# Optimization experiments

Measured on AMD Instinct MI355X. Metric: run time of the kernel, lower is better.

Reference implementation:

```python
import math
import jax, jax.numpy as jnp
import numpy as np

GROUPS = 8
EPS = 1e-5


def setup_inputs() -> dict:
    key = jax.random.key(0)
    ks = jax.random.split(key, 4)
    B, C, H, W = 4, 128, 64, 64
    x = jax.random.normal(ks[0], (B, C, H, W), dtype=jnp.float32)
    norm_w = jnp.ones((C,), dtype=jnp.float32)
    norm_b = jnp.zeros((C,), dtype=jnp.float32)
    qkv_w = jax.random.normal(ks[1], (3 * C, C), dtype=jnp.float32) * 0.02
    qkv_b = jnp.zeros((3 * C,), dtype=jnp.float32)
    proj_w = jax.random.normal(ks[2], (C, C), dtype=jnp.float32) * 0.02
    proj_b = jnp.zeros((C,), dtype=jnp.float32)
    return {"x": x, "norm_w": norm_w, "norm_b": norm_b,
            "qkv_w": qkv_w, "qkv_b": qkv_b,
            "proj_w": proj_w, "proj_b": proj_b}


def reference(x, norm_w, norm_b, qkv_w, qkv_b, proj_w, proj_b):
    B, C, H, W = x.shape
    N = H * W
    # GroupNorm over (C/G, H, W) per group
    xr = x.reshape(B, GROUPS, C // GROUPS, N)
    mean = xr.mean(axis=(2, 3), keepdims=True)
    var = xr.var(axis=(2, 3), keepdims=True)
    h = ((xr - mean) * jax.lax.rsqrt(var + EPS)).reshape(B, C, N)
    h = h * norm_w[None, :, None] + norm_b[None, :, None]
    # 1x1 conv QKV == per-pixel linear: [B, 3C, N]
    qkv = jnp.einsum('oc,bcn->bon', qkv_w, h) + qkv_b[None, :, None]
    q, k, v = jnp.split(qkv, 3, axis=1)  # each [B, C, N]
    scale = 1.0 / math.sqrt(C)
    attn = jax.nn.softmax(jnp.einsum('bci,bcj->bij', q, k) * scale, axis=-1)  # [B,N,N]
    out = jnp.einsum('bij,bcj->bci', attn, v)  # [B, C, N]
    proj = jnp.einsum('oc,bcn->bon', proj_w, out) + proj_b[None, :, None]
    return x + proj.reshape(B, C, H, W)
```

## Files before the change

kernel.cpp:

```cpp
#include <hip/hip_runtime.h>

typedef float  f32x4   __attribute__((ext_vector_type(4)));
typedef float  f32x16  __attribute__((ext_vector_type(16)));
typedef short  bf16x8  __attribute__((ext_vector_type(8)));
typedef unsigned short u16;

constexpr int B_ = 4;
constexpr int C_ = 128;
constexpr int N_ = 4096;
constexpr int G_ = 8;
constexpr int CperG = 16;
constexpr float EPS_ = 1e-5f;
constexpr float SCALE_ = 0.08838834764831845f;

__device__ inline u16 f2bf(float f) {
    union { float f; unsigned u; } v; v.f = f;
    unsigned r = v.u + 0x7fffu + ((v.u >> 16) & 1u);
    return (u16)(r >> 16);
}
__device__ inline unsigned pk2(float a, float b) {
    return (unsigned)f2bf(a) | ((unsigned)f2bf(b) << 16);
}

__global__ __launch_bounds__(256) void prep_kernel(const float* __restrict__ x,
                                                   const float* __restrict__ qw,
                                                   const float* __restrict__ pw,
                                                   float* __restrict__ stats2,
                                                   u16* __restrict__ qwbf,
                                                   u16* __restrict__ pwbf) {
    int blk = blockIdx.x;
    if (blk < 256) {
        __shared__ float rs[4], rss[4];
        int bg = blk >> 3, chunk = blk & 7;
        const float4* xp = (const float4*)(x + (size_t)bg * (CperG * N_)) + chunk * 2048;
        float s = 0.f, ss = 0.f;
        for (int i = threadIdx.x; i < 2048; i += 256) {
            float4 v = xp[i];
            s  += v.x + v.y + v.z + v.w;
            ss += v.x*v.x + v.y*v.y + v.z*v.z + v.w*v.w;
        }
        #pragma unroll
        for (int off = 32; off > 0; off >>= 1) {
            s  += __shfl_down(s, off);
            ss += __shfl_down(ss, off);
        }
        int wv = threadIdx.x >> 6, ln = threadIdx.x & 63;
        if (ln == 0) { rs[wv] = s; rss[wv] = ss; }
        __syncthreads();
        if (threadIdx.x == 0) {
            stats2[blk*2]     = rs[0] + rs[1] + rs[2] + rs[3];
            stats2[blk*2 + 1] = rss[0] + rss[1] + rss[2] + rss[3];
        }
    } else {
        int fidx = ((blk - 256) * 256 + threadIdx.x) * 4;
        float4 v;
        u16* dst;
        if (fidx < 3*C_*C_) { v = *(const float4*)(qw + fidx); dst = qwbf + fidx; }
        else { int j = fidx - 3*C_*C_; v = *(const float4*)(pw + j); dst = pwbf + j; }
        ushort4 o;
        o.x = f2bf(v.x); o.y = f2bf(v.y); o.z = f2bf(v.z); o.w = f2bf(v.w);
        *(ushort4*)dst = o;
    }
}

constexpr int HS = 136;

__global__ __launch_bounds__(256, 2) void qkv_kernel(const float* __restrict__ x,
                                                     const float* __restrict__ stats2,
                                                     const float* __restrict__ nw,
                                                     const float* __restrict__ nb,
                                                     const u16* __restrict__ qwbf,
                                                     const float* __restrict__ qb,
                                                     u16* __restrict__ Qt,
                                                     u16* __restrict__ Ksw,
                                                     u16* __restrict__ Vsw,
                                                     float* __restrict__ qn2,
                                                     int* __restrict__ kmaxI) {
    int n0 = (blockIdx.x & 63) * 64;
    int b  = blockIdx.x >> 6;
    __shared__ u16 hs[64 * HS];
    __shared__ u16 Wl[64 * HS];
    __shared__ float gmean[8], grstd[8];
    int t = threadIdx.x;
    const float invM = 1.f / (float)(CperG * N_);
    if (t < 8) {
        const float* sp = stats2 + (size_t)(b*G_ + t)*16;
        float S = 0.f, SS = 0.f;
        #pragma unroll
        for (int k2 = 0; k2 < 8; ++k2) { S += sp[k2*2]; SS += sp[k2*2 + 1]; }
        float mean = S * invM;
        gmean[t] = mean;
        grstd[t] = rsqrtf(SS * invM - mean*mean + EPS_);
    }
    __syncthreads();
    #pragma unroll
    for (int r = 0; r < 8; ++r) {
        int idx = t + (r << 8);
        int c = idx >> 4, n4 = idx & 15;
        int g = c >> 4;
        float wgt = nw[c] * grstd[g];
        float bia = nb[c] - gmean[g] * wgt;
        float4 xv = *(const float4*)(x + ((size_t)(b*C_ + c))*N_ + n0 + n4*4);
        int base = (n4*4) * HS + c;
        hs[base         ] = f2bf(xv.x*wgt + bia);
        hs[base +     HS] = f2bf(xv.y*wgt + bia);
        hs[base + 2 * HS] = f2bf(xv.z*wgt + bia);
        hs[base + 3 * HS] = f2bf(xv.w*wgt + bia);
    }
    __syncthreads();
    int w = t >> 6, lane = t & 63, lo = lane & 15, hi = lane >> 4;
    bf16x8 hf[4];
    #pragma unroll
    for (int ch = 0; ch < 4; ++ch)
        hf[ch] = *(const bf16x8*)(hs + (16*w + lo)*HS + 32*ch + 8*hi);

    int Tb = (n0 >> 5) + (w >> 1);
    float nq = 0.f, nk = 0.f;
    for (int ck = 0; ck < 6; ++ck) {
        {
            int r = t >> 2, p = t & 3;
            const u16* src = qwbf + (size_t)(ck*64 + r)*C_ + p*32;
            u16* dst = Wl + r*HS + p*32;
            #pragma unroll
            for (int k2 = 0; k2 < 4; ++k2)
                *(uint4*)(dst + 8*k2) = *(const uint4*)(src + 8*k2);
        }
        __syncthreads();
        #pragma unroll
        for (int ot = 0; ot < 4; ++ot) {
            int o16 = ck*64 + ot*16;
            bf16x8 wf[4];
            #pragma unroll
            for (int ch = 0; ch < 4; ++ch)
                wf[ch] = *(const bf16x8*)(Wl + (ot*16 + lo)*HS + 32*ch + 8*hi);
            if (o16 < 2*C_) {
                f32x4 acc = (f32x4){0.f, 0.f, 0.f, 0.f};
                #pragma unroll
                for (int ch = 0; ch < 4; ++ch)
                    acc = __builtin_amdgcn_mfma_f32_16x16x32_bf16(wf[ch], hf[ch], acc, 0, 0, 0);
                float4 bv = *(const float4*)(qb + o16 + 4*hi);
                int n = n0 + 16*w + lo;
                ushort4 o4;
                if (o16 < C_) {
                    float q0 = (acc[0] + bv.x) * SCALE_;
                    float q1 = (acc[1] + bv.y) * SCALE_;
                    float q2 = (acc[2] + bv.z) * SCALE_;
                    float q3 = (acc[3] + bv.w) * SCALE_;
                    nq += (q0*q0 + q1*q1) + (q2*q2 + q3*q3);
                    o4.x = f2bf(q0); o4.y = f2bf(q1); o4.z = f2bf(q2); o4.w = f2bf(q3);
                    *(ushort4*)(Qt + ((size_t)b*N_ + n)*C_ + o16 + 4*hi) = o4;
                } else {
                    float k0 = acc[0] + bv.x, k1 = acc[1] + bv.y;
                    float k2 = acc[2] + bv.z, k3 = acc[3] + bv.w;
                    nk += (k0*k0 + k1*k1) + (k2*k2 + k3*k3);
                    o4.x = f2bf(k0); o4.y = f2bf(k1); o4.z = f2bf(k2); o4.w = f2bf(k3);
                    int cc = (o16 - C_) >> 4;
                    int lp = (16*(w & 1) + lo) + 32*(hi >> 1);
                    size_t fb = ((size_t)(b*128 + Tb)*8 + cc)*512;
                    *(ushort4*)(Ksw + fb + lp*8 + 4*(hi & 1)) = o4;
                }
            } else {
                f32x4 acc = (f32x4){0.f, 0.f, 0.f, 0.f};
                #pragma unroll
                for (int ch = 0; ch < 4; ++ch)
                    acc = __builtin_amdgcn_mfma_f32_16x16x32_bf16(hf[ch], wf[ch], acc, 0, 0, 0);
                float bia = qb[o16 + lo];
                ushort4 o4;
                o4.x = f2bf(acc[0] + bia);
                o4.y = f2bf(acc[1] + bia);
                o4.z = f2bf(acc[2] + bia);
                o4.w = f2bf(acc[3] + bia);
                int m  = (o16 - 2*C_) >> 4;
                int ct = m >> 1;
                int lp = (16*(m & 1) + lo) + 32*(hi & 1);
                size_t fb = (((size_t)(b*4 + ct)*128 + Tb)*2 + (w & 1))*512;
                *(ushort4*)(Vsw + fb + lp*8 + 4*(hi >> 1)) = o4;
            }
        }
        __syncthreads();
    }
    nq += __shfl_xor(nq, 16); nq += __shfl_xor(nq, 32);
    nk += __shfl_xor(nk, 16); nk += __shfl_xor(nk, 32);
    if (lane < 16) qn2[(size_t)b*N_ + n0 + 16*w + lo] = nq;
    #pragma unroll
    for (int off = 1; off < 16; off <<= 1)
        nk = fmaxf(nk, __shfl_xor(nk, off));
    if (lane == 0) atomicMax(&kmaxI[b], __float_as_int(nk));
}

__global__ __launch_bounds__(512, 2) void attn_kernel(const u16* __restrict__ Qt,
                                                      const u16* __restrict__ Ksw,
                                                      const u16* __restrict__ Vsw,
                                                      const float* __restrict__ qn2,
                                                      const int* __restrict__ kmaxI,
                                                      const u16* __restrict__ pwbf,
                                                      const float* __restrict__ pb,
                                                      const float* __restrict__ x,
                                                      float* __restrict__ out) {
    int lb = blockIdx.x;
    int b  = lb & 3;
    int i0 = 64 * (lb >> 2);
    int t = threadIdx.x;
    int w = t >> 6, lane = t & 63;
    int l31 = lane & 31, h = lane >> 5;
    int qt = w >> 2, ks = w & 3;

    __shared__ float Ob[64 * 132];
    __shared__ float lW[8][32];

    float kmax = sqrtf(__int_as_float(kmaxI[b]));
    float mq = sqrtf(qn2[(size_t)b*N_ + i0 + 32*qt + l31]) * kmax * 1.02f + 1e-6f;

    const u16* Qb = Qt + (size_t)b*N_*C_;
    bf16x8 qf[8];
    #pragma unroll
    for (int cc = 0; cc < 8; ++cc)
        qf[cc] = *(const bf16x8*)(Qb + (size_t)(i0 + 32*qt + l31)*C_ + 16*cc + 8*h);

    f32x16 acc[4];
    #pragma unroll
    for (int ct = 0; ct < 4; ++ct)
        #pragma unroll
        for (int r = 0; r < 16; ++r) acc[ct][r] = 0.f;
    float psum = 0.f;

    const u16* Kbase = Ksw + ((size_t)(b*128 + ks*32)*8)*512;
    bf16x8 kf[8], kn[8];
    #pragma unroll
    for (int cc = 0; cc < 8; ++cc)
        kf[cc] = *(const bf16x8*)(Kbase + cc*512 + lane*8);

    for (int it = 0; it < 32; ++it) {
        f32x16 s;
        #pragma unroll
        for (int r = 0; r < 16; ++r) s[r] = 0.f;
        #pragma unroll
        for (int cc = 0; cc < 8; ++cc)
            s = __builtin_amdgcn_mfma_f32_32x32x16_bf16(kf[cc], qf[cc], s, 0, 0, 0);
        {
            const u16* Kn = Kbase + ((size_t)(((it + 1) & 31))*8)*512;
            #pragma unroll
            for (int cc = 0; cc < 8; ++cc)
                kn[cc] = *(const bf16x8*)(Kn + cc*512 + lane*8);
        }
        int T = ks*32 + it;
        bf16x8 v1[4], v2[4];
        #pragma unroll
        for (int ct = 0; ct < 4; ++ct) {
            const u16* vb = Vsw + (((size_t)(b*4 + ct)*128 + T)*2)*512;
            v1[ct] = *(const bf16x8*)(vb + lane*8);
            v2[ct] = *(const bf16x8*)(vb + 512 + lane*8);
        }
        float p[16];
        #pragma unroll
        for (int r = 0; r < 16; ++r) {
            p[r] = __expf(s[r] - mq);
            psum += p[r];
        }
        union { bf16x8 v; unsigned u[4]; } pf1, pf2;
        pf1.u[0] = pk2(p[0],  p[1]);  pf1.u[1] = pk2(p[2],  p[3]);
        pf1.u[2] = pk2(p[4],  p[5]);  pf1.u[3] = pk2(p[6],  p[7]);
        pf2.u[0] = pk2(p[8],  p[9]);  pf2.u[1] = pk2(p[10], p[11]);
        pf2.u[2] = pk2(p[12], p[13]); pf2.u[3] = pk2(p[14], p[15]);
        #pragma unroll
        for (int ct = 0; ct < 4; ++ct) {
            acc[ct] = __builtin_amdgcn_mfma_f32_32x32x16_bf16(v1[ct], pf1.v, acc[ct], 0, 0, 0);
            acc[ct] = __builtin_amdgcn_mfma_f32_32x32x16_bf16(v2[ct], pf2.v, acc[ct], 0, 0, 0);
        }
        #pragma unroll
        for (int cc = 0; cc < 8; ++cc) kf[cc] = kn[cc];
    }

    psum += __shfl_xor(psum, 32);
    if (lane < 32) lW[w][l31] = psum;
    for (int i = 0; i < 4; ++i) {
        if (ks == i) {
            int q = 32*qt + l31;
            #pragma unroll
            for (int ct = 0; ct < 4; ++ct)
                #pragma unroll
                for (int qd = 0; qd < 4; ++qd) {
                    int c = 32*ct + 8*qd + 4*h;
                    float4 vv;
                    vv.x = acc[ct][4*qd + 0];
                    vv.y = acc[ct][4*qd + 1];
                    vv.z = acc[ct][4*qd + 2];
                    vv.w = acc[ct][4*qd + 3];
                    if (i == 0) {
                        *(float4*)(Ob + q*132 + c) = vv;
                    } else {
                        float4 o = *(const float4*)(Ob + q*132 + c);
                        o.x += vv.x; o.y += vv.y; o.z += vv.z; o.w += vv.w;
                        *(float4*)(Ob + q*132 + c) = o;
                    }
                }
        }
        __syncthreads();
    }
    int lo = lane & 15, hi = lane >> 4;
    int qtile = w >> 1, os = w & 1;
    int q = 16*qtile + lo;
    int qg = 4*(q >> 5), qc = q & 31;
    float linv = 1.f / (lW[qg][qc] + lW[qg+1][qc] + lW[qg+2][qc] + lW[qg+3][qc]);
    bf16x8 aa[4];
    #pragma unroll
    for (int ch = 0; ch < 4; ++ch) {
        float4 ua = *(const float4*)(Ob + q*132 + 32*ch + 8*hi);
        float4 ub = *(const float4*)(Ob + q*132 + 32*ch + 8*hi + 4);
        union { bf16x8 hh; unsigned u[4]; } pkd;
        pkd.u[0] = pk2(ua.x*linv, ua.y*linv);
        pkd.u[1] = pk2(ua.z*linv, ua.w*linv);
        pkd.u[2] = pk2(ub.x*linv, ub.y*linv);
        pkd.u[3] = pk2(ub.z*linv, ub.w*linv);
        aa[ch] = pkd.hh;
    }
    #pragma unroll
    for (int ot = 0; ot < 4; ++ot) {
        int ob = 64*os + 16*ot;
        f32x4 pr = (f32x4){0.f, 0.f, 0.f, 0.f};
        #pragma unroll
        for (int ch = 0; ch < 4; ++ch) {
            bf16x8 bw = *(const bf16x8*)(pwbf + (size_t)(ob + lo)*C_ + 32*ch + 8*hi);
            pr = __builtin_amdgcn_mfma_f32_16x16x32_bf16(aa[ch], bw, pr, 0, 0, 0);
        }
        int o = ob + lo;
        float pbv = pb[o];
        size_t base = ((size_t)(b*C_ + o))*N_ + i0 + 16*qtile + 4*hi;
        float4 xr = *(const float4*)(x + base);
        float4 res;
        res.x = xr.x + pr[0] + pbv;
        res.y = xr.y + pr[1] + pbv;
        res.z = xr.z + pr[2] + pbv;
        res.w = xr.w + pr[3] + pbv;
        *(float4*)(out + base) = res;
    }
}

extern "C" void kernel_launch(void* const* d_in, const int* in_sizes, int n_in,
                              void* d_out, int out_size, void* d_ws, size_t ws_size,
                              hipStream_t stream) {
    const float* x  = (const float*)d_in[0];
    const float* nw = (const float*)d_in[1];
    const float* nb = (const float*)d_in[2];
    const float* qw = (const float*)d_in[3];
    const float* qb = (const float*)d_in[4];
    const float* pw = (const float*)d_in[5];
    const float* pb = (const float*)d_in[6];
    float* out = (float*)d_out;

    char* p = (char*)d_ws;
    float* stats2 = (float*)p;                 p += 2048;
    float* qn2    = (float*)p;                 p += (size_t)B_*N_*4;
    int*   kmaxI  = (int*)p;                   p += 256;
    u16*   qwbf   = (u16*)p;                   p += (size_t)3*C_*C_*2;
    u16*   pwbf   = (u16*)p;                   p += (size_t)C_*C_*2;
    u16*   Qt     = (u16*)p;                   p += (size_t)B_*N_*C_*2;
    u16*   Ksw    = (u16*)p;                   p += (size_t)B_*N_*C_*2;
    u16*   Vsw    = (u16*)p;

    prep_kernel<<<dim3(320), 256, 0, stream>>>(x, qw, pw, stats2, qwbf, pwbf);
    qkv_kernel<<<dim3(256), 256, 0, stream>>>(x, stats2, nw, nb, qwbf, qb,
                                              Qt, Ksw, Vsw, qn2, kmaxI);
    attn_kernel<<<dim3(256), 512, 0, stream>>>(Qt, Ksw, Vsw, qn2, kmaxI,
                                               pwbf, pb, x, out);
}
```

Measured before the change: 153.9 us.

## Split QKV projection across sections, prefetch V, use hardware bf16 pack and exp2

```diff
diff --git a/kernel.cpp b/kernel.cpp
--- a/kernel.cpp
+++ b/kernel.cpp
@@ -11,15 +11,17 @@
 constexpr int G_ = 8;
 constexpr int CperG = 16;
 constexpr float EPS_ = 1e-5f;
-constexpr float SCALE_ = 0.08838834764831845f;
+constexpr float SCALE2_ = 0.08838834764831845f * 1.4426950408889634f;
 
 __device__ inline u16 f2bf(float f) {
     union { float f; unsigned u; } v; v.f = f;
     unsigned r = v.u + 0x7fffu + ((v.u >> 16) & 1u);
     return (u16)(r >> 16);
 }
-__device__ inline unsigned pk2(float a, float b) {
-    return (unsigned)f2bf(a) | ((unsigned)f2bf(b) << 16);
+__device__ inline unsigned cvtpk(float lo, float hi) {
+    unsigned r;
+    asm("v_cvt_pk_bf16_f32 %0, %1, %2" : "=v"(r) : "v"(lo), "v"(hi));
+    return r;
 }
 
 __global__ __launch_bounds__(256) void prep_kernel(const float* __restrict__ x,
@@ -65,7 +67,7 @@
 
 constexpr int HS = 136;
 
-__global__ __launch_bounds__(256, 2) void qkv_kernel(const float* __restrict__ x,
+__global__ __launch_bounds__(256, 3) void qkv_kernel(const float* __restrict__ x,
                                                      const float* __restrict__ stats2,
                                                      const float* __restrict__ nw,
                                                      const float* __restrict__ nb,
@@ -76,8 +78,10 @@
                                                      u16* __restrict__ Vsw,
                                                      float* __restrict__ qn2,
                                                      int* __restrict__ kmaxI) {
-    int n0 = (blockIdx.x & 63) * 64;
-    int b  = blockIdx.x >> 6;
+    int blk = blockIdx.x & 255;
+    int sec = blockIdx.x >> 8;
+    int n0 = (blk & 63) * 64;
+    int b  = blk >> 6;
     __shared__ u16 hs[64 * HS];
     __shared__ u16 Wl[64 * HS];
     __shared__ float gmean[8], grstd[8];
@@ -102,10 +106,12 @@
         float bia = nb[c] - gmean[g] * wgt;
         float4 xv = *(const float4*)(x + ((size_t)(b*C_ + c))*N_ + n0 + n4*4);
         int base = (n4*4) * HS + c;
-        hs[base         ] = f2bf(xv.x*wgt + bia);
-        hs[base +     HS] = f2bf(xv.y*wgt + bia);
-        hs[base + 2 * HS] = f2bf(xv.z*wgt + bia);
-        hs[base + 3 * HS] = f2bf(xv.w*wgt + bia);
+        unsigned u01 = cvtpk(xv.x*wgt + bia, xv.y*wgt + bia);
+        unsigned u23 = cvtpk(xv.z*wgt + bia, xv.w*wgt + bia);
+        hs[base         ] = (u16)(u01 & 0xffffu);
+        hs[base +     HS] = (u16)(u01 >> 16);
+        hs[base + 2 * HS] = (u16)(u23 & 0xffffu);
+        hs[base + 3 * HS] = (u16)(u23 >> 16);
     }
     __syncthreads();
     int w = t >> 6, lane = t & 63, lo = lane & 15, hi = lane >> 4;
@@ -116,7 +122,8 @@
 
     int Tb = (n0 >> 5) + (w >> 1);
     float nq = 0.f, nk = 0.f;
-    for (int ck = 0; ck < 6; ++ck) {
+    for (int ckj = 0; ckj < 2; ++ckj) {
+        int ck = 2*sec + ckj;
         {
             int r = t >> 2, p = t & 3;
             const u16* src = qwbf + (size_t)(ck*64 + r)*C_ + p*32;
@@ -140,24 +147,27 @@
                     acc = __builtin_amdgcn_mfma_f32_16x16x32_bf16(wf[ch], hf[ch], acc, 0, 0, 0);
                 float4 bv = *(const float4*)(qb + o16 + 4*hi);
                 int n = n0 + 16*w + lo;
-                ushort4 o4;
                 if (o16 < C_) {
-                    float q0 = (acc[0] + bv.x) * SCALE_;
-                    float q1 = (acc[1] + bv.y) * SCALE_;
-                    float q2 = (acc[2] + bv.z) * SCALE_;
-                    float q3 = (acc[3] + bv.w) * SCALE_;
+                    float q0 = (acc[0] + bv.x) * SCALE2_;
+                    float q1 = (acc[1] + bv.y) * SCALE2_;
+                    float q2 = (acc[2] + bv.z) * SCALE2_;
+                    float q3 = (acc[3] + bv.w) * SCALE2_;
                     nq += (q0*q0 + q1*q1) + (q2*q2 + q3*q3);
-                    o4.x = f2bf(q0); o4.y = f2bf(q1); o4.z = f2bf(q2); o4.w = f2bf(q3);
-                    *(ushort4*)(Qt + ((size_t)b*N_ + n)*C_ + o16 + 4*hi) = o4;
+                    union { ushort4 s4; unsigned u[2]; } o4;
+                    o4.u[0] = cvtpk(q0, q1);
+                    o4.u[1] = cvtpk(q2, q3);
+                    *(ushort4*)(Qt + ((size_t)b*N_ + n)*C_ + o16 + 4*hi) = o4.s4;
                 } else {
                     float k0 = acc[0] + bv.x, k1 = acc[1] + bv.y;
                     float k2 = acc[2] + bv.z, k3 = acc[3] + bv.w;
                     nk += (k0*k0 + k1*k1) + (k2*k2 + k3*k3);
-                    o4.x = f2bf(k0); o4.y = f2bf(k1); o4.z = f2bf(k2); o4.w = f2bf(k3);
+                    union { ushort4 s4; unsigned u[2]; } o4;
+                    o4.u[0] = cvtpk(k0, k1);
+                    o4.u[1] = cvtpk(k2, k3);
                     int cc = (o16 - C_) >> 4;
                     int lp = (16*(w & 1) + lo) + 32*(hi >> 1);
                     size_t fb = ((size_t)(b*128 + Tb)*8 + cc)*512;
-                    *(ushort4*)(Ksw + fb + lp*8 + 4*(hi & 1)) = o4;
+                    *(ushort4*)(Ksw + fb + lp*8 + 4*(hi & 1)) = o4.s4;
                 }
             } else {
                 f32x4 acc = (f32x4){0.f, 0.f, 0.f, 0.f};
@@ -165,27 +175,28 @@
                 for (int ch = 0; ch < 4; ++ch)
                     acc = __builtin_amdgcn_mfma_f32_16x16x32_bf16(hf[ch], wf[ch], acc, 0, 0, 0);
                 float bia = qb[o16 + lo];
-                ushort4 o4;
-                o4.x = f2bf(acc[0] + bia);
-                o4.y = f2bf(acc[1] + bia);
-                o4.z = f2bf(acc[2] + bia);
-                o4.w = f2bf(acc[3] + bia);
+                union { ushort4 s4; unsigned u[2]; } o4;
+                o4.u[0] = cvtpk(acc[0] + bia, acc[1] + bia);
+                o4.u[1] = cvtpk(acc[2] + bia, acc[3] + bia);
                 int m  = (o16 - 2*C_) >> 4;
                 int ct = m >> 1;
                 int lp = (16*(m & 1) + lo) + 32*(hi & 1);
                 size_t fb = (((size_t)(b*4 + ct)*128 + Tb)*2 + (w & 1))*512;
-                *(ushort4*)(Vsw + fb + lp*8 + 4*(hi >> 1)) = o4;
+                *(ushort4*)(Vsw + fb + lp*8 + 4*(hi >> 1)) = o4.s4;
             }
         }
         __syncthreads();
     }
-    nq += __shfl_xor(nq, 16); nq += __shfl_xor(nq, 32);
-    nk += __shfl_xor(nk, 16); nk += __shfl_xor(nk, 32);
-    if (lane < 16) qn2[(size_t)b*N_ + n0 + 16*w + lo] = nq;
-    #pragma unroll
-    for (int off = 1; off < 16; off <<= 1)
-        nk = fmaxf(nk, __shfl_xor(nk, off));
-    if (lane == 0) atomicMax(&kmaxI[b], __float_as_int(nk));
+    if (sec == 0) {
+        nq += __shfl_xor(nq, 16); nq += __shfl_xor(nq, 32);
+        if (lane < 16) qn2[(size_t)b*N_ + n0 + 16*w + lo] = nq;
+    } else if (sec == 1) {
+        nk += __shfl_xor(nk, 16); nk += __shfl_xor(nk, 32);
+        #pragma unroll
+        for (int off = 1; off < 16; off <<= 1)
+            nk = fmaxf(nk, __shfl_xor(nk, off));
+        if (lane == 0) atomicMax(&kmaxI[b], __float_as_int(nk));
+    }
 }
 
 __global__ __launch_bounds__(512, 2) void attn_kernel(const u16* __restrict__ Qt,
@@ -222,13 +233,20 @@
     for (int ct = 0; ct < 4; ++ct)
         #pragma unroll
         for (int r = 0; r < 16; ++r) acc[ct][r] = 0.f;
-    float psum = 0.f;
+    float ps0 = 0.f, ps1 = 0.f, ps2 = 0.f, ps3 = 0.f;
 
     const u16* Kbase = Ksw + ((size_t)(b*128 + ks*32)*8)*512;
     bf16x8 kf[8], kn[8];
     #pragma unroll
     for (int cc = 0; cc < 8; ++cc)
         kf[cc] = *(const bf16x8*)(Kbase + cc*512 + lane*8);
+    bf16x8 v1[4], v2[4], w1[4], w2[4];
+    #pragma unroll
+    for (int ct = 0; ct < 4; ++ct) {
+        const u16* vb = Vsw + (((size_t)(b*4 + ct)*128 + ks*32)*2)*512;
+        v1[ct] = *(const bf16x8*)(vb + lane*8);
+        v2[ct] = *(const bf16x8*)(vb + 512 + lane*8);
+    }
 
     for (int it = 0; it < 32; ++it) {
         f32x16 s;
@@ -237,31 +255,36 @@
         #pragma unroll
         for (int cc = 0; cc < 8; ++cc)
             s = __builtin_amdgcn_mfma_f32_32x32x16_bf16(kf[cc], qf[cc], s, 0, 0, 0);
+        int itn = (it + 1) & 31;
         {
-            const u16* Kn = Kbase + ((size_t)(((it + 1) & 31))*8)*512;
+            const u16* Kn = Kbase + ((size_t)itn*8)*512;
             #pragma unroll
             for (int cc = 0; cc < 8; ++cc)
                 kn[cc] = *(const bf16x8*)(Kn + cc*512 + lane*8);
         }
-        int T = ks*32 + it;
-        bf16x8 v1[4], v2[4];
-        #pragma unroll
-        for (int ct = 0; ct < 4; ++ct) {
-            const u16* vb = Vsw + (((size_t)(b*4 + ct)*128 + T)*2)*512;
-            v1[ct] = *(const bf16x8*)(vb + lane*8);
-            v2[ct] = *(const bf16x8*)(vb + 512 + lane*8);
+        {
+            int Tn = ks*32 + itn;
+            #pragma unroll
+            for (int ct = 0; ct < 4; ++ct) {
+                const u16* vb = Vsw + (((size_t)(b*4 + ct)*128 + Tn)*2)*512;
+                w1[ct] = *(const bf16x8*)(vb + lane*8);
+                w2[ct] = *(const bf16x8*)(vb + 512 + lane*8);
+            }
         }
         float p[16];
         #pragma unroll
-        for (int r = 0; r < 16; ++r) {
-            p[r] = __expf(s[r] - mq);
-            psum += p[r];
+        for (int r = 0; r < 16; ++r)
+            p[r] = __builtin_amdgcn_exp2f(s[r] - mq);
+        #pragma unroll
+        for (int r = 0; r < 16; r += 4) {
+            ps0 += p[r];     ps1 += p[r + 1];
+            ps2 += p[r + 2]; ps3 += p[r + 3];
         }
         union { bf16x8 v; unsigned u[4]; } pf1, pf2;
-        pf1.u[0] = pk2(p[0],  p[1]);  pf1.u[1] = pk2(p[2],  p[3]);
-        pf1.u[2] = pk2(p[4],  p[5]);  pf1.u[3] = pk2(p[6],  p[7]);
-        pf2.u[0] = pk2(p[8],  p[9]);  pf2.u[1] = pk2(p[10], p[11]);
-        pf2.u[2] = pk2(p[12], p[13]); pf2.u[3] = pk2(p[14], p[15]);
+        pf1.u[0] = cvtpk(p[0],  p[1]);  pf1.u[1] = cvtpk(p[2],  p[3]);
+        pf1.u[2] = cvtpk(p[4],  p[5]);  pf1.u[3] = cvtpk(p[6],  p[7]);
+        pf2.u[0] = cvtpk(p[8],  p[9]);  pf2.u[1] = cvtpk(p[10], p[11]);
+        pf2.u[2] = cvtpk(p[12], p[13]); pf2.u[3] = cvtpk(p[14], p[15]);
         #pragma unroll
         for (int ct = 0; ct < 4; ++ct) {
             acc[ct] = __builtin_amdgcn_mfma_f32_32x32x16_bf16(v1[ct], pf1.v, acc[ct], 0, 0, 0);
@@ -269,8 +292,11 @@
         }
         #pragma unroll
         for (int cc = 0; cc < 8; ++cc) kf[cc] = kn[cc];
-    }
-
+        #pragma unroll
+        for (int ct = 0; ct < 4; ++ct) { v1[ct] = w1[ct]; v2[ct] = w2[ct]; }
+    }
+
+    float psum = (ps0 + ps1) + (ps2 + ps3);
     psum += __shfl_xor(psum, 32);
     if (lane < 32) lW[w][l31] = psum;
     for (int i = 0; i < 4; ++i) {
@@ -308,10 +334,10 @@
         float4 ua = *(const float4*)(Ob + q*132 + 32*ch + 8*hi);
         float4 ub = *(const float4*)(Ob + q*132 + 32*ch + 8*hi + 4);
         union { bf16x8 hh; unsigned u[4]; } pkd;
-        pkd.u[0] = pk2(ua.x*linv, ua.y*linv);
-        pkd.u[1] = pk2(ua.z*linv, ua.w*linv);
-        pkd.u[2] = pk2(ub.x*linv, ub.y*linv);
-        pkd.u[3] = pk2(ub.z*linv, ub.w*linv);
+        pkd.u[0] = cvtpk(ua.x*linv, ua.y*linv);
+        pkd.u[1] = cvtpk(ua.z*linv, ua.w*linv);
+        pkd.u[2] = cvtpk(ub.x*linv, ub.y*linv);
+        pkd.u[3] = cvtpk(ub.z*linv, ub.w*linv);
         aa[ch] = pkd.hh;
     }
     #pragma unroll
@@ -359,7 +385,7 @@
     u16*   Vsw    = (u16*)p;
 
     prep_kernel<<<dim3(320), 256, 0, stream>>>(x, qw, pw, stats2, qwbf, pwbf);
-    qkv_kernel<<<dim3(256), 256, 0, stream>>>(x, stats2, nw, nb, qwbf, qb,
+    qkv_kernel<<<dim3(768), 256, 0, stream>>>(x, stats2, nw, nb, qwbf, qb,
                                               Qt, Ksw, Vsw, qn2, kmaxI);
     attn_kernel<<<dim3(256), 512, 0, stream>>>(Qt, Ksw, Vsw, qn2, kmaxI,
                                                pwbf, pb, x, out);
```

Measured after the change: 149.2 us (median of 2 runs). 3.1% less time.
